# Performance work log

Hardware: AMD Instinct MI355X
Metric: run time of the kernel (lower is better)

The kernel has to match this reference:

```python
import jax, jax.numpy as jnp
import numpy as np

NUM_HEADS = 8
RADIUS = 127          # local_attention_radius -> block_length = 128
RMAX = 64             # rel_pos_max_distance -> R = 2*RMAX+1 = 129


def setup_inputs() -> dict:
    key = jax.random.key(0)
    ks = jax.random.split(key, 9)
    B, S, D = 2, 4096, 512
    hd = D // NUM_HEADS
    R = 2 * RMAX + 1
    w = lambda k, shape: 0.02 * jax.random.normal(k, shape, jnp.float32)
    return {
        "Q": jax.random.normal(ks[0], (B, S, D), jnp.float32),
        "K": jax.random.normal(ks[1], (B, S, D), jnp.float32),
        "V": jax.random.normal(ks[2], (B, S, D), jnp.float32),
        "segment_ids": jnp.zeros((B, S), jnp.int32),
        "Wq": w(ks[3], (D, D)),
        "Wk": w(ks[4], (D, D)),
        "Wv": w(ks[5], (D, D)),
        "Wo": w(ks[6], (D, D)),
        "rel_emb": w(ks[7], (NUM_HEADS, R, hd)),
    }


def reference(Q, K, V, segment_ids, Wq, Wk, Wv, Wo, rel_emb):
    B, S, D = Q.shape
    h = NUM_HEADS
    hd = D // h
    bl = RADIUS + 1                      # block length
    nb = -(-S // bl)                     # num query blocks
    pad = nb * bl - S                    # 0 for S divisible by bl
    norm = float(hd) ** 0.5

    def proj(X, W):  # B x S x D -> B x h x S x hd
        return (X @ W).reshape(B, S, h, hd).transpose(0, 2, 1, 3)

    q = proj(Q, Wq)
    k = proj(K, Wk)
    v = proj(V, Wv)

    # query blocks: B x h x nb x bl x hd
    qb = jnp.pad(q, ((0, 0), (0, 0), (0, pad), (0, 0))).reshape(B, h, nb, bl, hd)
    # sliding key/value blocks: pad bl on each side, gather 3*bl window per block
    kp = jnp.pad(k, ((0, 0), (0, 0), (bl, bl + pad), (0, 0)))
    vp = jnp.pad(v, ((0, 0), (0, 0), (bl, bl + pad), (0, 0)))
    slid = jnp.arange(3 * bl)[None, :] + bl * jnp.arange(nb)[:, None]  # nb x 3bl
    kb = kp[:, :, slid, :]  # B x h x nb x 3bl x hd
    vb = vp[:, :, slid, :]

    energy = jnp.einsum("bhnqd,bhnkd->bhnqk", qb, kb)  # B x h x nb x bl x 3bl

    # relative position bias: Q @ rel_embeds^T then gather by rel pos ids
    qrel = jnp.einsum("bhnqd,hrd->bhnqr", qb, rel_emb)  # B x h x nb x bl x R
    i = jnp.arange(bl)
    j = jnp.arange(3 * bl)
    dpos = j[None, :] - bl - i[:, None]                 # bl x 3bl, key - query offset
    ids = jnp.clip(dpos, -RMAX, RMAX) + RMAX            # bl x 3bl in [0, 2*RMAX]
    rel_shift = qrel[:, :, :, i[:, None], ids]          # B x h x nb x bl x 3bl

    energy = (energy + rel_shift) / norm

    # mask: out-of-sequence keys and keys beyond local radius
    kg = bl * jnp.arange(nb)[:, None, None] + (j - bl)[None, None, :]
    invalid = (kg < 0) | (kg >= S) | (jnp.abs(dpos)[None] > RADIUS)    # nb x bl x 3bl
    energy = jnp.where(invalid[None, None], -jnp.inf, energy)

    attn = jax.nn.softmax(energy, axis=-1)
    outb = jnp.einsum("bhnqk,bhnkd->bhnqd", attn, vb)   # B x h x nb x bl x hd
    out = outb.reshape(B, h, nb * bl, hd)[:, :, :S, :]  # B x h x S x hd
    # torch code interleaves features as (head_dim, head): permute(0,2,3,1).flatten(2,3)
    out = out.transpose(0, 2, 3, 1).reshape(B, S, hd * h)
    return out @ Wo
```

## Files before the change

kernel.cpp:

```cpp
#include <hip/hip_runtime.h>
#include <hip/hip_bf16.h>

typedef unsigned short u16;
typedef __bf16 bf16_t;
typedef bf16_t bf16x8 __attribute__((ext_vector_type(8)));
typedef float f32x4 __attribute__((ext_vector_type(4)));
typedef u16 u16x4 __attribute__((ext_vector_type(4)));
typedef u16 u16x8 __attribute__((ext_vector_type(8)));

#define S_LEN 4096
#define NH 8
#define HD 64
#define DM 512
#define NB 32

__device__ __forceinline__ u16 f2bf(float f) {
  unsigned int u = __builtin_bit_cast(unsigned int, f);
  u = (u + 0x7fff + ((u >> 16) & 1)) >> 16;
  return (u16)u;
}
__device__ __forceinline__ float bf2f(u16 h) {
  unsigned int u = ((unsigned int)h) << 16;
  return __builtin_bit_cast(float, u);
}

#define GLDS16(gaddr, laddr)                                                  \
  __builtin_amdgcn_global_load_lds(                                           \
      (const __attribute__((address_space(1))) unsigned int*)(gaddr),         \
      (__attribute__((address_space(3))) unsigned int*)(laddr), 16, 0, 0)

__global__ __launch_bounds__(256) void conv_w(
    const float* __restrict__ Wq, const float* __restrict__ Wk,
    const float* __restrict__ Wv, const float* __restrict__ Wo,
    u16* __restrict__ WqT, u16* __restrict__ WkT, u16* __restrict__ WvT,
    u16* __restrict__ WoT) {
  const int z = blockIdx.y;
  const float* src = z == 0 ? Wq : (z == 1 ? Wk : (z == 2 ? Wv : Wo));
  u16* dst = z == 0 ? WqT : (z == 1 ? WkT : (z == 2 ? WvT : WoT));
  const float scl = (z == 0) ? 0.125f : 1.f;
  const int idx4 = blockIdx.x * 256 + threadIdx.x;
  const int nrow = idx4 >> 7;
  const int kbase = (idx4 & 127) * 4;
  u16x4 o;
#pragma unroll
  for (int j = 0; j < 4; ++j) {
    const int k = kbase + j;
    const int srow = (z == 3) ? ((k & 63) * 8 + (k >> 6)) : k;
    o[j] = f2bf(src[srow * DM + nrow] * scl);
  }
  *(u16x4*)(dst + nrow * DM + kbase) = o;
}

__global__ __launch_bounds__(128) void conv_rel(const float* __restrict__ rel,
                                                u16* __restrict__ relb) {
  const int e = (blockIdx.x * 128 + threadIdx.x) * 4;
  const int h = e / (129 * 64);
  const int rem = e - h * (129 * 64);
  const float4 v = *(const float4*)(rel + e);
  u16x4 o;
  o[0] = f2bf(v.x); o[1] = f2bf(v.y); o[2] = f2bf(v.z); o[3] = f2bf(v.w);
  *(u16x4*)(relb + (size_t)h * (144 * 64) + rem) = o;
}

template <int MODE>
__global__ __launch_bounds__(256, 4) void gemm_bf16(
    const float* __restrict__ Af0, const float* __restrict__ Af1,
    const float* __restrict__ Af2, const u16* __restrict__ Ab,
    const u16* __restrict__ B0, const u16* __restrict__ B1,
    const u16* __restrict__ B2, u16* __restrict__ C0, u16* __restrict__ C1,
    u16* __restrict__ C2, float* __restrict__ Cf) {
  __shared__ u16 As[2][64 * 32];
  __shared__ u16 Bs[2][128 * 32];

  const int z = blockIdx.z;
  const float* Af = (MODE == 1) ? (z == 0 ? Af0 : (z == 1 ? Af1 : Af2)) : 0;
  const u16* Bt = (MODE == 1) ? (z == 0 ? B0 : (z == 1 ? B1 : B2)) : B0;
  u16* Cb = (MODE == 1) ? (z == 0 ? C0 : (z == 1 ? C1 : C2)) : (u16*)0;

  const int tid = threadIdx.x;
  const int lane = tid & 63;
  const int w = tid >> 6;
  const int bm = blockIdx.x * 64;
  const int bn = blockIdx.y * 128;

  f32x4 acc[2][4];
#pragma unroll
  for (int mf = 0; mf < 2; ++mf)
#pragma unroll
    for (int nf = 0; nf < 4; ++nf) acc[mf][nf] = f32x4{0.f, 0.f, 0.f, 0.f};

  const int wr = w >> 1, wc = w & 1;
  const int lrow = lane & 15;
  const int lk = (lane >> 4) * 8;

  const int arow = tid >> 2;
  const int ac8 = (tid & 3) * 8;
  const long aoff = (long)(bm + arow) * DM + ac8;

  auto stageB = [&](int buf, int k0) {
#pragma unroll
    for (int c = 0; c < 2; ++c) {
      const int brow = bn + c * 64 + w * 16 + (lane >> 2);
      GLDS16(Bt + (long)brow * DM + k0 + (lane & 3) * 8,
             &Bs[buf][c * 2048 + w * 512]);
    }
  };
  auto stageA2 = [&](int buf, int k0) {
    const int r = bm + w * 16 + (lane >> 2);
    const int b = r >> 12, s = r & 4095;
    const int k = k0 + (lane & 3) * 8;
    GLDS16(Ab + ((long)((b * 8 + (k >> 6)) * 4096 + s)) * 64 + (k & 63),
           &As[buf][w * 512]);
  };
  auto writeA = [&](int buf, float4 x0, float4 x1) {
    u16x8 o;
    o[0] = f2bf(x0.x); o[1] = f2bf(x0.y); o[2] = f2bf(x0.z); o[3] = f2bf(x0.w);
    o[4] = f2bf(x1.x); o[5] = f2bf(x1.y); o[6] = f2bf(x1.z); o[7] = f2bf(x1.w);
    *(u16x8*)&As[buf][arow * 32 + ac8] = o;
  };

  auto compute = [&](int cur) {
    bf16x8 af[2], bfr[4];
#pragma unroll
    for (int mf = 0; mf < 2; ++mf)
      af[mf] = *(const bf16x8*)&As[cur][(wr * 32 + mf * 16 + lrow) * 32 + lk];
#pragma unroll
    for (int nf = 0; nf < 4; ++nf)
      bfr[nf] = *(const bf16x8*)&Bs[cur][(wc * 64 + nf * 16 + lrow) * 32 + lk];
#pragma unroll
    for (int mf = 0; mf < 2; ++mf)
#pragma unroll
      for (int nf = 0; nf < 4; ++nf)
        acc[mf][nf] = __builtin_amdgcn_mfma_f32_16x16x32_bf16(
            bfr[nf], af[mf], acc[mf][nf], 0, 0, 0);
  };

  if constexpr (MODE == 1) {
    float4 c0 = *(const float4*)&Af[aoff];
    float4 c1 = *(const float4*)&Af[aoff + 4];
    stageB(0, 0);
    writeA(0, c0, c1);
    __syncthreads();
    for (int t = 0; t < 16; ++t) {
      const int cur = t & 1;
      float4 n0, n1;
      if (t < 15) {
        n0 = *(const float4*)&Af[aoff + (t + 1) * 32];
        n1 = *(const float4*)&Af[aoff + (t + 1) * 32 + 4];
        stageB(cur ^ 1, (t + 1) * 32);
      }
      compute(cur);
      if (t < 15) writeA(cur ^ 1, n0, n1);
      __syncthreads();
    }
  } else {
    stageA2(0, 0);
    stageB(0, 0);
    __syncthreads();
    for (int t = 0; t < 16; ++t) {
      const int cur = t & 1;
      if (t < 15) {
        stageA2(cur ^ 1, (t + 1) * 32);
        stageB(cur ^ 1, (t + 1) * 32);
      }
      compute(cur);
      __syncthreads();
    }
  }

  const int lr4 = (lane >> 4) * 4;
  const int lc = lane & 15;
#pragma unroll
  for (int mf = 0; mf < 2; ++mf) {
    const int r = bm + wr * 32 + mf * 16 + lc;
    const int bi = r >> 12, s = r & 4095;
#pragma unroll
    for (int nf = 0; nf < 4; ++nf) {
      const int cg = bn + wc * 64 + nf * 16 + lr4;
      if (MODE == 1) {
        u16x4 o;
#pragma unroll
        for (int j = 0; j < 4; ++j) o[j] = f2bf(acc[mf][nf][j]);
        *(u16x4*)&Cb[((long)((bi * 8 + (cg >> 6)) * 4096 + s)) * 64 +
                     (cg & 63)] = o;
      } else {
        float4 o;
        o.x = acc[mf][nf][0]; o.y = acc[mf][nf][1];
        o.z = acc[mf][nf][2]; o.w = acc[mf][nf][3];
        *(float4*)&Cf[(long)r * DM + cg] = o;
      }
    }
  }
}

__global__ __launch_bounds__(256, 2) void attn_mfma(
    const u16* __restrict__ qg, const u16* __restrict__ kgl,
    const u16* __restrict__ vgl, const u16* __restrict__ relb,
    u16* __restrict__ pre) {
  const int n = blockIdx.x, hh = blockIdx.y, b = blockIdx.z;
  const int tid = threadIdx.x;
  const int lane = tid & 63, w = tid >> 6;
  const int g = lane >> 4, lc = lane & 15;

  __shared__ u16 Ks[64 * 72];
  __shared__ u16 Vt[64 * 72];
  __shared__ u16 Pl[4][32 * 72];
  __shared__ u16 qrelL[128 * 132];

  const size_t bh = (size_t)(b * NH + hh);

  const u16* qbase = qg + (bh * S_LEN + (size_t)n * 128 + w * 32) * HD;
  bf16x8 qf[2][2];
#pragma unroll
  for (int qt = 0; qt < 2; ++qt)
#pragma unroll
    for (int dc = 0; dc < 2; ++dc)
      qf[qt][dc] =
          *(const bf16x8*)(qbase + (lc + 16 * qt) * HD + g * 8 + 32 * dc);

  const u16* rh = relb + (size_t)hh * (144 * 64);
#pragma unroll
  for (int rt = 0; rt < 9; ++rt) {
    f32x4 acc[2] = {{0.f, 0.f, 0.f, 0.f}, {0.f, 0.f, 0.f, 0.f}};
#pragma unroll
    for (int dc = 0; dc < 2; ++dc) {
      const bf16x8 rf =
          *(const bf16x8*)(rh + (lc + 16 * rt) * 64 + g * 8 + 32 * dc);
#pragma unroll
      for (int qt = 0; qt < 2; ++qt)
        acc[qt] = __builtin_amdgcn_mfma_f32_16x16x32_bf16(qf[qt][dc], rf,
                                                          acc[qt], 0, 0, 0);
    }
#pragma unroll
    for (int qt = 0; qt < 2; ++qt)
#pragma unroll
      for (int jj = 0; jj < 4; ++jj)
        qrelL[(w * 32 + qt * 16 + g * 4 + jj) * 132 + lc + 16 * rt] =
            f2bf(acc[qt][jj]);
  }

  float m_r[2][4], l_r[2][4];
  f32x4 Oa[2][4];
#pragma unroll
  for (int qt = 0; qt < 2; ++qt)
#pragma unroll
    for (int jj = 0; jj < 4; ++jj) {
      m_r[qt][jj] = -1e30f;
      l_r[qt][jj] = 0.f;
    }
#pragma unroll
  for (int qt = 0; qt < 2; ++qt)
#pragma unroll
    for (int dt = 0; dt < 4; ++dt) Oa[qt][dt] = f32x4{0.f, 0.f, 0.f, 0.f};

  const u16* kbase = kgl + bh * S_LEN * HD;
  const u16* vbase = vgl + bh * S_LEN * HD;
  const int sk = tid & 63;
  const int sd = (tid >> 6) * 16;

  const int t0 = (n == 0) ? 2 : 0;
  const int t1 = (n == NB - 1) ? 4 : 6;

  for (int t = t0; t < t1; ++t) {
    {
      const int kglob = n * 128 - 128 + t * 64 + sk;
      const int kc = min(max(kglob, 0), S_LEN - 1);
      const u16* krow = kbase + (size_t)kc * HD + sd;
      const u16* vrow = vbase + (size_t)kc * HD + sd;
      const u16x8 ka = *(const u16x8*)krow;
      const u16x8 kb2 = *(const u16x8*)(krow + 8);
      const u16x8 va = *(const u16x8*)vrow;
      const u16x8 vb2 = *(const u16x8*)(vrow + 8);
      *(u16x8*)&Ks[sk * 72 + sd] = ka;
      *(u16x8*)&Ks[sk * 72 + sd + 8] = kb2;
#pragma unroll
      for (int e = 0; e < 8; ++e) {
        Vt[(sd + e) * 72 + sk] = va[e];
        Vt[(sd + 8 + e) * 72 + sk] = vb2[e];
      }
    }
    __syncthreads();

    f32x4 E[2][4];
#pragma unroll
    for (int qt = 0; qt < 2; ++qt)
#pragma unroll
      for (int kt = 0; kt < 4; ++kt) E[qt][kt] = f32x4{0.f, 0.f, 0.f, 0.f};
#pragma unroll
    for (int kt = 0; kt < 4; ++kt)
#pragma unroll
      for (int dc = 0; dc < 2; ++dc) {
        const bf16x8 kf =
            *(const bf16x8*)&Ks[(lc + 16 * kt) * 72 + g * 8 + 32 * dc];
#pragma unroll
        for (int qt = 0; qt < 2; ++qt)
          E[qt][kt] = __builtin_amdgcn_mfma_f32_16x16x32_bf16(
              qf[qt][dc], kf, E[qt][kt], 0, 0, 0);
      }

#pragma unroll
    for (int qt = 0; qt < 2; ++qt)
#pragma unroll
      for (int jj = 0; jj < 4; ++jj) {
        const int q = w * 32 + qt * 16 + g * 4 + jj;
#pragma unroll
        for (int kt = 0; kt < 4; ++kt) {
          const int j = t * 64 + kt * 16 + lc;
          const int dpos = j - 128 - q;
          const int kglob = n * 128 - 128 + j;
          const int idc = min(max(dpos, -64), 64) + 64;
          const float bias = bf2f(qrelL[q * 132 + idc]);
          const float e = E[qt][kt][jj] + bias;
          const bool bad = (dpos > 127) || (dpos < -127) ||
                           ((unsigned)kglob >= (unsigned)S_LEN);
          E[qt][kt][jj] = bad ? -1e30f : e;
        }
      }

#pragma unroll
    for (int qt = 0; qt < 2; ++qt)
#pragma unroll
      for (int jj = 0; jj < 4; ++jj) {
        float mx = fmaxf(fmaxf(E[qt][0][jj], E[qt][1][jj]),
                         fmaxf(E[qt][2][jj], E[qt][3][jj]));
        mx = fmaxf(mx, __shfl_xor(mx, 1));
        mx = fmaxf(mx, __shfl_xor(mx, 2));
        mx = fmaxf(mx, __shfl_xor(mx, 4));
        mx = fmaxf(mx, __shfl_xor(mx, 8));
        const float nm = fmaxf(m_r[qt][jj], mx);
        const float sc = __expf(m_r[qt][jj] - nm);
        m_r[qt][jj] = nm;
        l_r[qt][jj] *= sc;
#pragma unroll
        for (int dt = 0; dt < 4; ++dt) Oa[qt][dt][jj] *= sc;
        float ps = 0.f;
#pragma unroll
        for (int kt = 0; kt < 4; ++kt) {
          const float p = __expf(E[qt][kt][jj] - nm);
          ps += p;
          Pl[w][(qt * 16 + g * 4 + jj) * 72 + lc + 16 * kt] = f2bf(p);
        }
        ps += __shfl_xor(ps, 1);
        ps += __shfl_xor(ps, 2);
        ps += __shfl_xor(ps, 4);
        ps += __shfl_xor(ps, 8);
        l_r[qt][jj] += ps;
      }
    __syncthreads();

#pragma unroll
    for (int c = 0; c < 2; ++c) {
      bf16x8 pf[2];
#pragma unroll
      for (int qt = 0; qt < 2; ++qt)
        pf[qt] = *(const bf16x8*)&Pl[w][(lc + 16 * qt) * 72 + g * 8 + 32 * c];
#pragma unroll
      for (int dt = 0; dt < 4; ++dt) {
        const bf16x8 vf =
            *(const bf16x8*)&Vt[(lc + 16 * dt) * 72 + g * 8 + 32 * c];
#pragma unroll
        for (int qt = 0; qt < 2; ++qt)
          Oa[qt][dt] = __builtin_amdgcn_mfma_f32_16x16x32_bf16(
              pf[qt], vf, Oa[qt][dt], 0, 0, 0);
      }
    }
    __syncthreads();
  }

  u16* prow = pre + (bh * S_LEN + (size_t)n * 128 + w * 32) * HD;
#pragma unroll
  for (int qt = 0; qt < 2; ++qt)
#pragma unroll
    for (int jj = 0; jj < 4; ++jj) {
      const float inv = 1.f / l_r[qt][jj];
      const int row = qt * 16 + g * 4 + jj;
#pragma unroll
      for (int dt = 0; dt < 4; ++dt)
        prow[row * HD + lc + 16 * dt] = f2bf(Oa[qt][dt][jj] * inv);
    }
}

extern "C" void kernel_launch(void* const* d_in, const int* in_sizes, int n_in,
                              void* d_out, int out_size, void* d_ws,
                              size_t ws_size, hipStream_t stream) {
  const float* Q = (const float*)d_in[0];
  const float* K = (const float*)d_in[1];
  const float* V = (const float*)d_in[2];
  const float* Wq = (const float*)d_in[4];
  const float* Wk = (const float*)d_in[5];
  const float* Wv = (const float*)d_in[6];
  const float* Wo = (const float*)d_in[7];
  const float* rel = (const float*)d_in[8];
  float* out = (float*)d_out;

  const size_t NE = 4194304;
  u16* ws16 = (u16*)d_ws;
  u16* qb = ws16;
  u16* kb = qb + NE;
  u16* vb = kb + NE;
  u16* pre = vb + NE;
  u16* WqT = pre + NE;
  u16* WkT = WqT + 262144;
  u16* WvT = WkT + 262144;
  u16* WoT = WvT + 262144;
  u16* relb = WoT + 262144;

  conv_w<<<dim3(256, 4), 256, 0, stream>>>(Wq, Wk, Wv, Wo, WqT, WkT, WvT, WoT);
  conv_rel<<<dim3(129), 128, 0, stream>>>(rel, relb);
  gemm_bf16<1><<<dim3(128, 4, 3), 256, 0, stream>>>(
      Q, K, V, nullptr, WqT, WkT, WvT, qb, kb, vb, nullptr);
  attn_mfma<<<dim3(NB, NH, 2), 256, 0, stream>>>(qb, kb, vb, relb, pre);
  gemm_bf16<2><<<dim3(128, 4, 1), 256, 0, stream>>>(
      nullptr, nullptr, nullptr, pre, WoT, nullptr, nullptr, nullptr, nullptr,
      nullptr, out);
}
```

Measured before the change: 193.4 us.

## Triple-buffer GEMM with async fp32 A staging and tile-transpose weight conversion

The GEMM moves from a two-stage to a three-stage LDS pipeline with explicit vmcnt waits and raw barriers, and the projection GEMM now stages fp32 activations directly into LDS via global_load_lds. The fp32-to-bf16 conversion moves to fragment-load time using packed cvt instructions. This removes register round-trips and the synchronous global loads for A. The weight conversion kernel becomes an LDS-tiled transpose so global reads are coalesced. LDS use grows, so the occupancy hint drops to 3 blocks per CU.

```diff
diff --git a/kernel.cpp b/kernel.cpp
--- a/kernel.cpp
+++ b/kernel.cpp
@@ -38,17 +38,33 @@
   const float* src = z == 0 ? Wq : (z == 1 ? Wk : (z == 2 ? Wv : Wo));
   u16* dst = z == 0 ? WqT : (z == 1 ? WkT : (z == 2 ? WvT : WoT));
   const float scl = (z == 0) ? 0.125f : 1.f;
-  const int idx4 = blockIdx.x * 256 + threadIdx.x;
-  const int nrow = idx4 >> 7;
-  const int kbase = (idx4 & 127) * 4;
-  u16x4 o;
-#pragma unroll
-  for (int j = 0; j < 4; ++j) {
-    const int k = kbase + j;
+  const int k0 = (blockIdx.x >> 3) * 64;
+  const int n0 = (blockIdx.x & 7) * 64;
+
+  __shared__ u16 T[64][68];
+  const int rr = threadIdx.x >> 4;
+  const int c4 = (threadIdx.x & 15) * 4;
+
+#pragma unroll
+  for (int p = 0; p < 4; ++p) {
+    const int r = p * 16 + rr;
+    const int k = k0 + r;
     const int srow = (z == 3) ? ((k & 63) * 8 + (k >> 6)) : k;
-    o[j] = f2bf(src[srow * DM + nrow] * scl);
-  }
-  *(u16x4*)(dst + nrow * DM + kbase) = o;
+    const float4 v = *(const float4*)&src[srow * DM + n0 + c4];
+    u16x4 o;
+    o[0] = f2bf(v.x * scl); o[1] = f2bf(v.y * scl);
+    o[2] = f2bf(v.z * scl); o[3] = f2bf(v.w * scl);
+    *(u16x4*)&T[r][c4] = o;
+  }
+  __syncthreads();
+#pragma unroll
+  for (int p = 0; p < 4; ++p) {
+    const int nn = p * 16 + rr;
+    u16x4 o;
+#pragma unroll
+    for (int j = 0; j < 4; ++j) o[j] = T[c4 + j][nn];
+    *(u16x4*)&dst[(n0 + nn) * DM + k0 + c4] = o;
+  }
 }
 
 __global__ __launch_bounds__(128) void conv_rel(const float* __restrict__ rel,
@@ -63,14 +79,15 @@
 }
 
 template <int MODE>
-__global__ __launch_bounds__(256, 4) void gemm_bf16(
+__global__ __launch_bounds__(256, 3) void gemm_bf16(
     const float* __restrict__ Af0, const float* __restrict__ Af1,
     const float* __restrict__ Af2, const u16* __restrict__ Ab,
     const u16* __restrict__ B0, const u16* __restrict__ B1,
     const u16* __restrict__ B2, u16* __restrict__ C0, u16* __restrict__ C1,
     u16* __restrict__ C2, float* __restrict__ Cf) {
-  __shared__ u16 As[2][64 * 32];
-  __shared__ u16 Bs[2][128 * 32];
+  constexpr int ABYTES = (MODE == 1) ? 64 * 32 * 4 : 64 * 32 * 2;
+  __shared__ __align__(16) unsigned char AsRaw[3][ABYTES];
+  __shared__ __align__(16) u16 Bs[3][128 * 32];
 
   const int z = blockIdx.z;
   const float* Af = (MODE == 1) ? (z == 0 ? Af0 : (z == 1 ? Af1 : Af2)) : 0;
@@ -93,37 +110,58 @@
   const int lrow = lane & 15;
   const int lk = (lane >> 4) * 8;
 
-  const int arow = tid >> 2;
-  const int ac8 = (tid & 3) * 8;
-  const long aoff = (long)(bm + arow) * DM + ac8;
-
-  auto stageB = [&](int buf, int k0) {
-#pragma unroll
-    for (int c = 0; c < 2; ++c) {
-      const int brow = bn + c * 64 + w * 16 + (lane >> 2);
-      GLDS16(Bt + (long)brow * DM + k0 + (lane & 3) * 8,
-             &Bs[buf][c * 2048 + w * 512]);
+  auto stage = [&](int buf, int k0) {
+    if constexpr (MODE == 1) {
+#pragma unroll
+      for (int t = 0; t < 2; ++t) {
+        const int c = w * 2 + t;
+        GLDS16(Af + (long)(bm + c * 8 + (lane >> 3)) * DM + k0 + (lane & 7) * 4,
+               (float*)AsRaw[buf] + c * 256);
+        GLDS16(Bt + (long)(bn + c * 16 + (lane >> 2)) * DM + k0 + (lane & 3) * 8,
+               &Bs[buf][c * 512]);
+      }
+    } else {
+      {
+        const int c = w;
+        const int r = bm + c * 16 + (lane >> 2);
+        const int b = r >> 12, s = r & 4095;
+        const int k = k0 + (lane & 3) * 8;
+        GLDS16(Ab + ((long)((b * 8 + (k >> 6)) * 4096 + s)) * 64 + (k & 63),
+               (u16*)AsRaw[buf] + c * 512);
+      }
+#pragma unroll
+      for (int t = 0; t < 2; ++t) {
+        const int c = w * 2 + t;
+        GLDS16(Bt + (long)(bn + c * 16 + (lane >> 2)) * DM + k0 + (lane & 3) * 8,
+               &Bs[buf][c * 512]);
+      }
     }
   };
-  auto stageA2 = [&](int buf, int k0) {
-    const int r = bm + w * 16 + (lane >> 2);
-    const int b = r >> 12, s = r & 4095;
-    const int k = k0 + (lane & 3) * 8;
-    GLDS16(Ab + ((long)((b * 8 + (k >> 6)) * 4096 + s)) * 64 + (k & 63),
-           &As[buf][w * 512]);
-  };
-  auto writeA = [&](int buf, float4 x0, float4 x1) {
-    u16x8 o;
-    o[0] = f2bf(x0.x); o[1] = f2bf(x0.y); o[2] = f2bf(x0.z); o[3] = f2bf(x0.w);
-    o[4] = f2bf(x1.x); o[5] = f2bf(x1.y); o[6] = f2bf(x1.z); o[7] = f2bf(x1.w);
-    *(u16x8*)&As[buf][arow * 32 + ac8] = o;
+
+  auto loadA = [&](int cur, int mf) -> bf16x8 {
+    if constexpr (MODE == 1) {
+      const float* p =
+          (const float*)AsRaw[cur] + (wr * 32 + mf * 16 + lrow) * 32 + lk;
+      const float4 a0 = *(const float4*)p;
+      const float4 a1 = *(const float4*)(p + 4);
+      unsigned int w0, w1, w2, w3;
+      asm("v_cvt_pk_bf16_f32 %0, %1, %2" : "=v"(w0) : "v"(a0.x), "v"(a0.y));
+      asm("v_cvt_pk_bf16_f32 %0, %1, %2" : "=v"(w1) : "v"(a0.z), "v"(a0.w));
+      asm("v_cvt_pk_bf16_f32 %0, %1, %2" : "=v"(w2) : "v"(a1.x), "v"(a1.y));
+      asm("v_cvt_pk_bf16_f32 %0, %1, %2" : "=v"(w3) : "v"(a1.z), "v"(a1.w));
+      union { unsigned int u[4]; bf16x8 v; } r;
+      r.u[0] = w0; r.u[1] = w1; r.u[2] = w2; r.u[3] = w3;
+      return r.v;
+    } else {
+      return *(const bf16x8*)((const u16*)AsRaw[cur] +
+                              (wr * 32 + mf * 16 + lrow) * 32 + lk);
+    }
   };
 
   auto compute = [&](int cur) {
     bf16x8 af[2], bfr[4];
 #pragma unroll
-    for (int mf = 0; mf < 2; ++mf)
-      af[mf] = *(const bf16x8*)&As[cur][(wr * 32 + mf * 16 + lrow) * 32 + lk];
+    for (int mf = 0; mf < 2; ++mf) af[mf] = loadA(cur, mf);
 #pragma unroll
     for (int nf = 0; nf < 4; ++nf)
       bfr[nf] = *(const bf16x8*)&Bs[cur][(wc * 64 + nf * 16 + lrow) * 32 + lk];
@@ -135,37 +173,21 @@
             bfr[nf], af[mf], acc[mf][nf], 0, 0, 0);
   };
 
-  if constexpr (MODE == 1) {
-    float4 c0 = *(const float4*)&Af[aoff];
-    float4 c1 = *(const float4*)&Af[aoff + 4];
-    stageB(0, 0);
-    writeA(0, c0, c1);
-    __syncthreads();
-    for (int t = 0; t < 16; ++t) {
-      const int cur = t & 1;
-      float4 n0, n1;
-      if (t < 15) {
-        n0 = *(const float4*)&Af[aoff + (t + 1) * 32];
-        n1 = *(const float4*)&Af[aoff + (t + 1) * 32 + 4];
-        stageB(cur ^ 1, (t + 1) * 32);
-      }
-      compute(cur);
-      if (t < 15) writeA(cur ^ 1, n0, n1);
-      __syncthreads();
-    }
-  } else {
-    stageA2(0, 0);
-    stageB(0, 0);
-    __syncthreads();
-    for (int t = 0; t < 16; ++t) {
-      const int cur = t & 1;
-      if (t < 15) {
-        stageA2(cur ^ 1, (t + 1) * 32);
-        stageB(cur ^ 1, (t + 1) * 32);
-      }
-      compute(cur);
-      __syncthreads();
-    }
+  stage(0, 0);
+  stage(1, 32);
+  for (int t = 0; t < 16; ++t) {
+    if (t < 15) {
+      if constexpr (MODE == 1)
+        asm volatile("s_waitcnt vmcnt(4)" ::: "memory");
+      else
+        asm volatile("s_waitcnt vmcnt(3)" ::: "memory");
+    } else {
+      asm volatile("s_waitcnt vmcnt(0)" ::: "memory");
+    }
+    __builtin_amdgcn_s_barrier();
+    __builtin_amdgcn_sched_barrier(0);
+    if (t < 14) stage((t + 2) % 3, (t + 2) * 32);
+    compute(t % 3);
   }
 
   const int lr4 = (lane >> 4) * 4;
@@ -405,7 +427,7 @@
   u16* WoT = WvT + 262144;
   u16* relb = WoT + 262144;
 
-  conv_w<<<dim3(256, 4), 256, 0, stream>>>(Wq, Wk, Wv, Wo, WqT, WkT, WvT, WoT);
+  conv_w<<<dim3(64, 4), 256, 0, stream>>>(Wq, Wk, Wv, Wo, WqT, WkT, WvT, WoT);
   conv_rel<<<dim3(129), 128, 0, stream>>>(rel, relb);
   gemm_bf16<1><<<dim3(128, 4, 3), 256, 0, stream>>>(
       Q, K, V, nullptr, WqT, WkT, WvT, qb, kb, vb, nullptr);
```

Result: no change. 192.3 us (-0.6%).
